# Kernel tuning notes

Measured on AMD Instinct MI355X. Metric: run time of the kernel, lower is better.

Reference implementation:

```python
import jax, jax.numpy as jnp
import numpy as np

LOSS_ALPHA = 0.7  # Config.loss_alpha


def setup_inputs() -> dict:
    key = jax.random.key(0)
    k1, k2, k3 = jax.random.split(key, 3)
    N, D, K = 1024, 256, 65536
    online_emb = jax.random.normal(k1, (N, D), dtype=jnp.float32)
    mom_emb = jax.random.normal(k2, (N, D), dtype=jnp.float32)
    queue = jax.random.normal(k3, (D, K), dtype=jnp.float32)
    temp = jnp.full((1,), 0.07, dtype=jnp.float32)
    return {"online_emb": online_emb, "mom_emb": mom_emb, "queue": queue, "temp": temp}


def _ce_label0(logits):
    # cross-entropy with target class 0 for every row, mean over batch
    return jnp.mean(jax.nn.logsumexp(logits, axis=1) - logits[:, 0])


def reference(online_emb, mom_emb, queue, temp):
    pos_sim = jnp.einsum('nd,nd->n', online_emb, mom_emb)          # [N]
    neg_sim = jnp.einsum('nd,dk->nk', online_emb, queue)           # [N, K]
    logits_raw = jnp.concatenate([pos_sim[:, None], neg_sim], axis=1)  # [N, K+1]
    t = temp[0]
    loss_online = _ce_label0(logits_raw / t)
    loss_momentum = _ce_label0(logits_raw / jax.lax.stop_gradient(t))
    return LOSS_ALPHA * loss_online + (1.0 - LOSS_ALPHA) * loss_momentum
```

## Files before the change

### kernel.cpp

```cpp
#include <hip/hip_runtime.h>
#include <hip/hip_bf16.h>


#define NROWS 1024
#define DDIM  256
#define KQ    65536
#define BN    128
#define NPART 512
#define LN2_F 0.69314718055994531f

typedef short  short8  __attribute__((ext_vector_type(8)));
typedef float  floatx4 __attribute__((ext_vector_type(4)));

__device__ __forceinline__ unsigned short f2bf(float f) {
    unsigned int u = __float_as_uint(f);
    u += 0x7FFFu + ((u >> 16) & 1u);
    return (unsigned short)(u >> 16);
}

#define DPPMOV(x, ctrl) \
    __uint_as_float(__builtin_amdgcn_mov_dpp(__float_as_uint(x), (ctrl), 0xF, 0xF, true))

__device__ __forceinline__ float dpp16_max(float x) {
    x = fmaxf(x, DPPMOV(x, 0xB1));
    x = fmaxf(x, DPPMOV(x, 0x4E));
    x = fmaxf(x, DPPMOV(x, 0x141));
    x = fmaxf(x, DPPMOV(x, 0x140));
    return x;
}
__device__ __forceinline__ float dpp16_sum(float x) {
    x += DPPMOV(x, 0xB1);
    x += DPPMOV(x, 0x4E);
    x += DPPMOV(x, 0x141);
    x += DPPMOV(x, 0x140);
    return x;
}

__global__ __launch_bounds__(256)
void conv_a(const float* __restrict__ A, const float* __restrict__ temp,
            unsigned short* __restrict__ Ab, float* __restrict__ out)
{
    if (blockIdx.x == 0 && threadIdx.x == 0) out[0] = 0.0f;
    const float s = 1.0f / (temp[0] * LN2_F);
    const int i = blockIdx.x * 256 + threadIdx.x;
    const floatx4 v = ((const floatx4*)A)[i];
    ushort4 w;
    w.x = f2bf(v.x * s); w.y = f2bf(v.y * s);
    w.z = f2bf(v.z * s); w.w = f2bf(v.w * s);
    ((ushort4*)Ab)[i] = w;
}

__global__ __launch_bounds__(256, 2)
void gemm_softmax(const unsigned short* __restrict__ Ab,
                  const float* __restrict__ Q,
                  float2* __restrict__ partials)
{
    __shared__ __align__(16) unsigned short Bl[BN * DDIM];

    const int tid  = threadIdx.x;
    const int lane = tid & 63;
    const int wave = tid >> 6;
    const int l15  = lane & 15;
    const int quad = lane >> 4;
    const int nb   = blockIdx.x;
    const int nbase = nb * BN;

    #pragma unroll
    for (int iter = 0; iter < 4; ++iter) {
        const int t2 = iter * 256 + tid;
        const int ny = t2 & 31;
        const int ko = t2 >> 5;
        floatx4 v[8];
        #pragma unroll
        for (int j = 0; j < 8; ++j)
            v[j] = __builtin_nontemporal_load(
                       (const floatx4*)(Q + (size_t)(ko * 8 + j) * KQ + nbase + ny * 4));
        #pragma unroll
        for (int i2 = 0; i2 < 4; ++i2) {
            const int n = ny * 4 + i2;
            const int phys = ko ^ (n & 15);
            short8 w;
            #pragma unroll
            for (int j = 0; j < 8; ++j)
                w[j] = (short)f2bf(v[j][i2]);
            *(short8*)&Bl[n * DDIM + phys * 8] = w;
        }
    }
    __syncthreads();

    #pragma unroll 1
    for (int g = 0; g < 4; ++g) {
        const int rowbase = g * 256 + wave * 64;
        const unsigned short* apb = Ab + (size_t)(rowbase + l15) * DDIM + quad * 8;

        floatx4 acc[4][8] = {};
        short8 afA[4], afB[4], bfA[8], bfB[8];

        #pragma unroll
        for (int i = 0; i < 4; ++i)
            afA[i] = *(const short8*)(apb + i * 16 * DDIM);
        {
            const int vb = l15 * 512 + ((quad ^ l15) * 16);
            #pragma unroll
            for (int j = 0; j < 8; ++j)
                bfA[j] = *(const short8*)((const char*)Bl + vb + j * 8192);
        }

        #pragma unroll 1
        for (int sp = 0; sp < 4; ++sp) {
            const int s1 = 2 * sp + 1;
            #pragma unroll
            for (int i = 0; i < 4; ++i)
                afB[i] = *(const short8*)(apb + i * 16 * DDIM + s1 * 32);
            {
                const int vb = l15 * 512 + (((4 * s1 + quad) ^ l15) * 16);
                #pragma unroll
                for (int j = 0; j < 8; ++j)
                    bfB[j] = *(const short8*)((const char*)Bl + vb + j * 8192);
            }
            #pragma unroll
            for (int i = 0; i < 4; ++i)
                #pragma unroll
                for (int j = 0; j < 8; ++j)
                    acc[i][j] = __builtin_amdgcn_mfma_f32_16x16x32_bf16(afA[i], bfA[j], acc[i][j], 0, 0, 0);

            const int s2 = (2 * sp + 2) & 7;
            #pragma unroll
            for (int i = 0; i < 4; ++i)
                afA[i] = *(const short8*)(apb + i * 16 * DDIM + s2 * 32);
            {
                const int vb = l15 * 512 + (((4 * s2 + quad) ^ l15) * 16);
                #pragma unroll
                for (int j = 0; j < 8; ++j)
                    bfA[j] = *(const short8*)((const char*)Bl + vb + j * 8192);
            }
            #pragma unroll
            for (int i = 0; i < 4; ++i)
                #pragma unroll
                for (int j = 0; j < 8; ++j)
                    acc[i][j] = __builtin_amdgcn_mfma_f32_16x16x32_bf16(afB[i], bfB[j], acc[i][j], 0, 0, 0);
        }

        #pragma unroll
        for (int i = 0; i < 4; ++i) {
            float2 tmp[4];
            #pragma unroll
            for (int r = 0; r < 4; ++r) {
                float mx = acc[i][0][r];
                #pragma unroll
                for (int j = 1; j < 8; ++j) mx = fmaxf(mx, acc[i][j][r]);
                mx = dpp16_max(mx);
                float s2 = 0.f;
                #pragma unroll
                for (int j = 0; j < 8; ++j)
                    s2 += __builtin_amdgcn_exp2f(acc[i][j][r] - mx);
                s2 = dpp16_sum(s2);
                tmp[r] = make_float2(mx, s2);
            }
            if (l15 == 0) {
                const int row = rowbase + i * 16 + quad * 4;
                floatx4* dst = (floatx4*)(partials + (size_t)nb * NROWS + row);
                floatx4 w0 = {tmp[0].x, tmp[0].y, tmp[1].x, tmp[1].y};
                floatx4 w1 = {tmp[2].x, tmp[2].y, tmp[3].x, tmp[3].y};
                __builtin_nontemporal_store(w0, dst);
                __builtin_nontemporal_store(w1, dst + 1);
            }
        }
    }
}

__global__ __launch_bounds__(256)
void finalize_rows(const float2* __restrict__ partials,
                   const float* __restrict__ online,
                   const float* __restrict__ mom,
                   const float* __restrict__ temp,
                   float* __restrict__ out)
{
    const int t = threadIdx.x;
    __shared__ float2 sm[16][17];
    __shared__ float sm_pos[16];

    {
        const float s = 1.0f / (temp[0] * LN2_F);
        const int r2 = t >> 4, c2 = t & 15;
        const float* po = online + (size_t)(blockIdx.x * 16 + r2) * DDIM + c2 * 16;
        const float* pm = mom    + (size_t)(blockIdx.x * 16 + r2) * DDIM + c2 * 16;
        float d = 0.f;
        #pragma unroll
        for (int w = 0; w < 4; ++w) {
            const floatx4 a = *(const floatx4*)(po + w * 4);
            const floatx4 b = *(const floatx4*)(pm + w * 4);
            d += a.x * b.x + a.y * b.y + a.z * b.z + a.w * b.w;
        }
        d = dpp16_sum(d);
        if (c2 == 0) sm_pos[r2] = d * s;
    }

    const int rl  = t & 15;
    const int grp = t >> 4;
    const int row = blockIdx.x * 16 + rl;

    float M = -3.0e38f, S = 0.f;
    #pragma unroll 1
    for (int pb = 0; pb < 32; pb += 8) {
        float2 v[8];
        #pragma unroll
        for (int j = 0; j < 8; ++j)
            v[j] = partials[(size_t)(grp * 32 + pb + j) * NROWS + row];
        #pragma unroll
        for (int j = 0; j < 8; ++j) {
            const float M2 = fmaxf(M, v[j].x);
            S = S * __builtin_amdgcn_exp2f(M - M2) + v[j].y * __builtin_amdgcn_exp2f(v[j].x - M2);
            M = M2;
        }
    }
    sm[grp][rl] = make_float2(M, S);
    __syncthreads();

    if (t < 64) {
        float val = 0.f;
        if (t < 16) {
            float Mm = -3.0e38f, Ss = 0.f;
            #pragma unroll
            for (int g2 = 0; g2 < 16; ++g2) {
                const float2 v = sm[g2][t];
                const float M2 = fmaxf(Mm, v.x);
                Ss = Ss * __builtin_amdgcn_exp2f(Mm - M2) + v.y * __builtin_amdgcn_exp2f(v.x - M2);
                Mm = M2;
            }
            const float p  = sm_pos[t];
            const float M2 = fmaxf(Mm, p);
            const float L  = Ss * __builtin_amdgcn_exp2f(Mm - M2) + __builtin_amdgcn_exp2f(p - M2);
            val = (M2 + __builtin_amdgcn_logf(L) - p) * LN2_F;
        }
        val += __shfl_xor(val, 1, 64);
        val += __shfl_xor(val, 2, 64);
        val += __shfl_xor(val, 4, 64);
        val += __shfl_xor(val, 8, 64);
        val += __shfl_xor(val, 16, 64);
        val += __shfl_xor(val, 32, 64);
        if (t == 0) atomicAdd(out, val * (1.0f / (float)NROWS));
    }
}

extern "C" void kernel_launch(void* const* d_in, const int* in_sizes, int n_in,
                              void* d_out, int out_size, void* d_ws, size_t ws_size,
                              hipStream_t stream)
{
    const float* online = (const float*)d_in[0];
    const float* mom    = (const float*)d_in[1];
    const float* queue  = (const float*)d_in[2];
    const float* temp   = (const float*)d_in[3];
    float* out = (float*)d_out;

    char* ws = (char*)d_ws;
    unsigned short* Ab = (unsigned short*)ws;
    float2* partials   = (float2*)(ws + 524288);

    conv_a<<<256, 256, 0, stream>>>(online, temp, Ab, out);
    gemm_softmax<<<KQ / BN, 256, 0, stream>>>(Ab, queue, partials);
    finalize_rows<<<64, 256, 0, stream>>>(partials, online, mom, temp, out);
}
```

Baseline: 150.9 us.

## Switch to 32x32x16 MFMA with 64-column queue tiles and more blocks

Halves the queue tile width to 64 columns, doubling the grid to 1024 blocks and the partials count, and replaces the 16x16x32 MFMA tiling with 32x32x16 MFMA on 2x2 accumulator tiles per wave. The occupancy target rises to 3 blocks per CU, helped by less shared memory per block. The intent is better CU load balance and a cheaper per-wave fragment footprint. The trade-offs are twice as many partials for the finalize kernel to merge, extra cross-half shuffles in the softmax epilogue, and less B-tile reuse per block.

```diff
diff --git a/kernel.cpp b/kernel.cpp
--- a/kernel.cpp
+++ b/kernel.cpp
@@ -5,12 +5,13 @@
 #define NROWS 1024
 #define DDIM  256
 #define KQ    65536
-#define BN    128
-#define NPART 512
+#define BN    64
+#define NPART 1024
 #define LN2_F 0.69314718055994531f
 
-typedef short  short8  __attribute__((ext_vector_type(8)));
-typedef float  floatx4 __attribute__((ext_vector_type(4)));
+typedef short  short8   __attribute__((ext_vector_type(8)));
+typedef float  floatx4  __attribute__((ext_vector_type(4)));
+typedef float  floatx16 __attribute__((ext_vector_type(16)));
 
 __device__ __forceinline__ unsigned short f2bf(float f) {
     unsigned int u = __float_as_uint(f);
@@ -50,7 +51,7 @@
     ((ushort4*)Ab)[i] = w;
 }
 
-__global__ __launch_bounds__(256, 2)
+__global__ __launch_bounds__(256, 3)
 void gemm_softmax(const unsigned short* __restrict__ Ab,
                   const float* __restrict__ Q,
                   float2* __restrict__ partials)
@@ -60,16 +61,17 @@
     const int tid  = threadIdx.x;
     const int lane = tid & 63;
     const int wave = tid >> 6;
+    const int l31  = lane & 31;
     const int l15  = lane & 15;
-    const int quad = lane >> 4;
+    const int half = lane >> 5;
     const int nb   = blockIdx.x;
     const int nbase = nb * BN;
 
     #pragma unroll
-    for (int iter = 0; iter < 4; ++iter) {
+    for (int iter = 0; iter < 2; ++iter) {
         const int t2 = iter * 256 + tid;
-        const int ny = t2 & 31;
-        const int ko = t2 >> 5;
+        const int ny = t2 & 15;
+        const int ko = t2 >> 4;
         floatx4 v[8];
         #pragma unroll
         for (int j = 0; j < 8; ++j)
@@ -88,82 +90,78 @@
     }
     __syncthreads();
 
+    const int nA = l31 * 512;
+    const int nB = (32 + l31) * 512;
+
     #pragma unroll 1
     for (int g = 0; g < 4; ++g) {
         const int rowbase = g * 256 + wave * 64;
-        const unsigned short* apb = Ab + (size_t)(rowbase + l15) * DDIM + quad * 8;
-
-        floatx4 acc[4][8] = {};
-        short8 afA[4], afB[4], bfA[8], bfB[8];
-
-        #pragma unroll
-        for (int i = 0; i < 4; ++i)
-            afA[i] = *(const short8*)(apb + i * 16 * DDIM);
+        const unsigned short* apb = Ab + (size_t)(rowbase + l31) * DDIM + half * 8;
+
+        floatx16 acc[2][2] = {};
+        short8 afA[2], afB[2], bfA[2], bfB[2];
+
+        afA[0] = *(const short8*)(apb);
+        afA[1] = *(const short8*)(apb + 32 * DDIM);
         {
-            const int vb = l15 * 512 + ((quad ^ l15) * 16);
+            const int off = ((half ^ l15) * 16);
+            bfA[0] = *(const short8*)((const char*)Bl + nA + off);
+            bfA[1] = *(const short8*)((const char*)Bl + nB + off);
+        }
+
+        #pragma unroll 1
+        for (int sp = 0; sp < 8; ++sp) {
+            const int s1 = 2 * sp + 1;
+            afB[0] = *(const short8*)(apb + s1 * 16);
+            afB[1] = *(const short8*)(apb + 32 * DDIM + s1 * 16);
+            {
+                const int off = (((2 * s1 + half) ^ l15) * 16);
+                bfB[0] = *(const short8*)((const char*)Bl + nA + off);
+                bfB[1] = *(const short8*)((const char*)Bl + nB + off);
+            }
+            acc[0][0] = __builtin_amdgcn_mfma_f32_32x32x16_bf16(afA[0], bfA[0], acc[0][0], 0, 0, 0);
+            acc[0][1] = __builtin_amdgcn_mfma_f32_32x32x16_bf16(afA[0], bfA[1], acc[0][1], 0, 0, 0);
+            acc[1][0] = __builtin_amdgcn_mfma_f32_32x32x16_bf16(afA[1], bfA[0], acc[1][0], 0, 0, 0);
+            acc[1][1] = __builtin_amdgcn_mfma_f32_32x32x16_bf16(afA[1], bfA[1], acc[1][1], 0, 0, 0);
+
+            const int s2 = (2 * sp + 2) & 15;
+            afA[0] = *(const short8*)(apb + s2 * 16);
+            afA[1] = *(const short8*)(apb + 32 * DDIM + s2 * 16);
+            {
+                const int off = (((2 * s2 + half) ^ l15) * 16);
+                bfA[0] = *(const short8*)((const char*)Bl + nA + off);
+                bfA[1] = *(const short8*)((const char*)Bl + nB + off);
+            }
+            acc[0][0] = __builtin_amdgcn_mfma_f32_32x32x16_bf16(afB[0], bfB[0], acc[0][0], 0, 0, 0);
+            acc[0][1] = __builtin_amdgcn_mfma_f32_32x32x16_bf16(afB[0], bfB[1], acc[0][1], 0, 0, 0);
+            acc[1][0] = __builtin_amdgcn_mfma_f32_32x32x16_bf16(afB[1], bfB[0], acc[1][0], 0, 0, 0);
+            acc[1][1] = __builtin_amdgcn_mfma_f32_32x32x16_bf16(afB[1], bfB[1], acc[1][1], 0, 0, 0);
+        }
+
+        #pragma unroll
+        for (int ti = 0; ti < 2; ++ti) {
+            float2 vals[16];
             #pragma unroll
-            for (int j = 0; j < 8; ++j)
-                bfA[j] = *(const short8*)((const char*)Bl + vb + j * 8192);
-        }
-
-        #pragma unroll 1
-        for (int sp = 0; sp < 4; ++sp) {
-            const int s1 = 2 * sp + 1;
-            #pragma unroll
-            for (int i = 0; i < 4; ++i)
-                afB[i] = *(const short8*)(apb + i * 16 * DDIM + s1 * 32);
-            {
-                const int vb = l15 * 512 + (((4 * s1 + quad) ^ l15) * 16);
+            for (int reg = 0; reg < 16; ++reg) {
+                float mx = fmaxf(acc[ti][0][reg], acc[ti][1][reg]);
+                mx = dpp16_max(mx);
+                mx = fmaxf(mx, __shfl_xor(mx, 16, 64));
+                float s2 = __builtin_amdgcn_exp2f(acc[ti][0][reg] - mx)
+                         + __builtin_amdgcn_exp2f(acc[ti][1][reg] - mx);
+                s2 = dpp16_sum(s2);
+                s2 += __shfl_xor(s2, 16, 64);
+                vals[reg] = make_float2(mx, s2);
+            }
+            if (l31 == 0) {
+                const int rb0 = rowbase + ti * 32 + 4 * half;
+                float2* dst = partials + (size_t)nb * NROWS + rb0;
                 #pragma unroll
-                for (int j = 0; j < 8; ++j)
-                    bfB[j] = *(const short8*)((const char*)Bl + vb + j * 8192);
-            }
-            #pragma unroll
-            for (int i = 0; i < 4; ++i)
-                #pragma unroll
-                for (int j = 0; j < 8; ++j)
-                    acc[i][j] = __builtin_amdgcn_mfma_f32_16x16x32_bf16(afA[i], bfA[j], acc[i][j], 0, 0, 0);
-
-            const int s2 = (2 * sp + 2) & 7;
-            #pragma unroll
-            for (int i = 0; i < 4; ++i)
-                afA[i] = *(const short8*)(apb + i * 16 * DDIM + s2 * 32);
-            {
-                const int vb = l15 * 512 + (((4 * s2 + quad) ^ l15) * 16);
-                #pragma unroll
-                for (int j = 0; j < 8; ++j)
-                    bfA[j] = *(const short8*)((const char*)Bl + vb + j * 8192);
-            }
-            #pragma unroll
-            for (int i = 0; i < 4; ++i)
-                #pragma unroll
-                for (int j = 0; j < 8; ++j)
-                    acc[i][j] = __builtin_amdgcn_mfma_f32_16x16x32_bf16(afB[i], bfB[j], acc[i][j], 0, 0, 0);
-        }
-
-        #pragma unroll
-        for (int i = 0; i < 4; ++i) {
-            float2 tmp[4];
-            #pragma unroll
-            for (int r = 0; r < 4; ++r) {
-                float mx = acc[i][0][r];
-                #pragma unroll
-                for (int j = 1; j < 8; ++j) mx = fmaxf(mx, acc[i][j][r]);
-                mx = dpp16_max(mx);
-                float s2 = 0.f;
-                #pragma unroll
-                for (int j = 0; j < 8; ++j)
-                    s2 += __builtin_amdgcn_exp2f(acc[i][j][r] - mx);
-                s2 = dpp16_sum(s2);
-                tmp[r] = make_float2(mx, s2);
-            }
-            if (l15 == 0) {
-                const int row = rowbase + i * 16 + quad * 4;
-                floatx4* dst = (floatx4*)(partials + (size_t)nb * NROWS + row);
-                floatx4 w0 = {tmp[0].x, tmp[0].y, tmp[1].x, tmp[1].y};
-                floatx4 w1 = {tmp[2].x, tmp[2].y, tmp[3].x, tmp[3].y};
-                __builtin_nontemporal_store(w0, dst);
-                __builtin_nontemporal_store(w1, dst + 1);
+                for (int q = 0; q < 4; ++q) {
+                    floatx4 w0 = {vals[q*4+0].x, vals[q*4+0].y, vals[q*4+1].x, vals[q*4+1].y};
+                    floatx4 w1 = {vals[q*4+2].x, vals[q*4+2].y, vals[q*4+3].x, vals[q*4+3].y};
+                    __builtin_nontemporal_store(w0, (floatx4*)(dst + q * 8));
+                    __builtin_nontemporal_store(w1, (floatx4*)(dst + q * 8 + 2));
+                }
             }
         }
     }
@@ -202,11 +200,11 @@
 
     float M = -3.0e38f, S = 0.f;
     #pragma unroll 1
-    for (int pb = 0; pb < 32; pb += 8) {
+    for (int pb = 0; pb < 64; pb += 8) {
         float2 v[8];
         #pragma unroll
         for (int j = 0; j < 8; ++j)
-            v[j] = partials[(size_t)(grp * 32 + pb + j) * NROWS + row];
+            v[j] = partials[(size_t)(grp * 64 + pb + j) * NROWS + row];
         #pragma unroll
         for (int j = 0; j < 8; ++j) {
             const float M2 = fmaxf(M, v[j].x);
```

After: 186.5 us. 23.6% more time.

## Switch GEMM operands from bf16 to fp8 e4m3 with smaller key tiles

Applied to the files above, without the earlier changes.

Converts the scaled online embeddings and the queue tile to FP8 E4M3 instead of BF16, and uses fp8 MFMA instructions for the similarity GEMM. It halves the key tile (BN 64), which halves shared-memory use and allows four blocks per CU. The shared-memory swizzle is adapted to 8-byte fp8 fragments. Partials per row double, so the finalize kernel reduces twice as many chunks. FP8 sharply reduces mantissa precision of the logits, which risks going beyond the accuracy tolerance of the loss.

```diff
diff --git a/kernel.cpp b/kernel.cpp
--- a/kernel.cpp
+++ b/kernel.cpp
@@ -1,21 +1,20 @@
 #include <hip/hip_runtime.h>
 #include <hip/hip_bf16.h>
+#include <hip/hip_fp8.h>
 
 
 #define NROWS 1024
 #define DDIM  256
 #define KQ    65536
-#define BN    128
-#define NPART 512
+#define BN    64
+#define NPART 1024
 #define LN2_F 0.69314718055994531f
 
-typedef short  short8  __attribute__((ext_vector_type(8)));
-typedef float  floatx4 __attribute__((ext_vector_type(4)));
-
-__device__ __forceinline__ unsigned short f2bf(float f) {
-    unsigned int u = __float_as_uint(f);
-    u += 0x7FFFu + ((u >> 16) & 1u);
-    return (unsigned short)(u >> 16);
+typedef float floatx4 __attribute__((ext_vector_type(4)));
+
+__device__ __forceinline__ unsigned char f2e4(float f) {
+    __hip_fp8_e4m3 t(f);
+    return (unsigned char)t.__x;
 }
 
 #define DPPMOV(x, ctrl) \
@@ -38,24 +37,25 @@
 
 __global__ __launch_bounds__(256)
 void conv_a(const float* __restrict__ A, const float* __restrict__ temp,
-            unsigned short* __restrict__ Ab, float* __restrict__ out)
+            unsigned char* __restrict__ Ab, float* __restrict__ out)
 {
     if (blockIdx.x == 0 && threadIdx.x == 0) out[0] = 0.0f;
     const float s = 1.0f / (temp[0] * LN2_F);
     const int i = blockIdx.x * 256 + threadIdx.x;
     const floatx4 v = ((const floatx4*)A)[i];
-    ushort4 w;
-    w.x = f2bf(v.x * s); w.y = f2bf(v.y * s);
-    w.z = f2bf(v.z * s); w.w = f2bf(v.w * s);
-    ((ushort4*)Ab)[i] = w;
-}
-
-__global__ __launch_bounds__(256, 2)
-void gemm_softmax(const unsigned short* __restrict__ Ab,
+    unsigned int w = (unsigned int)f2e4(v.x * s)
+                   | ((unsigned int)f2e4(v.y * s) << 8)
+                   | ((unsigned int)f2e4(v.z * s) << 16)
+                   | ((unsigned int)f2e4(v.w * s) << 24);
+    ((unsigned int*)Ab)[i] = w;
+}
+
+__global__ __launch_bounds__(256, 4)
+void gemm_softmax(const unsigned char* __restrict__ Ab,
                   const float* __restrict__ Q,
                   float2* __restrict__ partials)
 {
-    __shared__ __align__(16) unsigned short Bl[BN * DDIM];
+    __shared__ __align__(16) unsigned char Bl[BN * DDIM];
 
     const int tid  = threadIdx.x;
     const int lane = tid & 63;
@@ -66,10 +66,10 @@
     const int nbase = nb * BN;
 
     #pragma unroll
-    for (int iter = 0; iter < 4; ++iter) {
+    for (int iter = 0; iter < 2; ++iter) {
         const int t2 = iter * 256 + tid;
-        const int ny = t2 & 31;
-        const int ko = t2 >> 5;
+        const int ny = t2 & 15;
+        const int ko = t2 >> 4;
         floatx4 v[8];
         #pragma unroll
         for (int j = 0; j < 8; ++j)
@@ -78,12 +78,12 @@
         #pragma unroll
         for (int i2 = 0; i2 < 4; ++i2) {
             const int n = ny * 4 + i2;
-            const int phys = ko ^ (n & 15);
-            short8 w;
+            const int phys = (ko & 16) | ((ko ^ n) & 15);
+            unsigned long w = 0;
             #pragma unroll
             for (int j = 0; j < 8; ++j)
-                w[j] = (short)f2bf(v[j][i2]);
-            *(short8*)&Bl[n * DDIM + phys * 8] = w;
+                w |= (unsigned long)f2e4(v[j][i2]) << (8 * j);
+            *(unsigned long*)&Bl[n * DDIM + phys * 8] = w;
         }
     }
     __syncthreads();
@@ -91,19 +91,19 @@
     #pragma unroll 1
     for (int g = 0; g < 4; ++g) {
         const int rowbase = g * 256 + wave * 64;
-        const unsigned short* apb = Ab + (size_t)(rowbase + l15) * DDIM + quad * 8;
-
-        floatx4 acc[4][8] = {};
-        short8 afA[4], afB[4], bfA[8], bfB[8];
+        const unsigned char* apb = Ab + (size_t)(rowbase + l15) * DDIM + quad * 8;
+
+        floatx4 acc[4][4] = {};
+        long afA[4], afB[4], bfA[4], bfB[4];
 
         #pragma unroll
         for (int i = 0; i < 4; ++i)
-            afA[i] = *(const short8*)(apb + i * 16 * DDIM);
+            afA[i] = *(const long*)(apb + i * 16 * DDIM);
         {
-            const int vb = l15 * 512 + ((quad ^ l15) * 16);
-            #pragma unroll
-            for (int j = 0; j < 8; ++j)
-                bfA[j] = *(const short8*)((const char*)Bl + vb + j * 8192);
+            const int phys = (quad & 16) | ((quad ^ l15) & 15);
+            #pragma unroll
+            for (int j = 0; j < 4; ++j)
+                bfA[j] = *(const long*)&Bl[(j * 16 + l15) * DDIM + phys * 8];
         }
 
         #pragma unroll 1
@@ -111,34 +111,36 @@
             const int s1 = 2 * sp + 1;
             #pragma unroll
             for (int i = 0; i < 4; ++i)
-                afB[i] = *(const short8*)(apb + i * 16 * DDIM + s1 * 32);
+                afB[i] = *(const long*)(apb + i * 16 * DDIM + s1 * 32);
             {
-                const int vb = l15 * 512 + (((4 * s1 + quad) ^ l15) * 16);
-                #pragma unroll
-                for (int j = 0; j < 8; ++j)
-                    bfB[j] = *(const short8*)((const char*)Bl + vb + j * 8192);
-            }
-            #pragma unroll
-            for (int i = 0; i < 4; ++i)
-                #pragma unroll
-                for (int j = 0; j < 8; ++j)
-                    acc[i][j] = __builtin_amdgcn_mfma_f32_16x16x32_bf16(afA[i], bfA[j], acc[i][j], 0, 0, 0);
+                const int c = 4 * s1 + quad;
+                const int phys = (c & 16) | ((c ^ l15) & 15);
+                #pragma unroll
+                for (int j = 0; j < 4; ++j)
+                    bfB[j] = *(const long*)&Bl[(j * 16 + l15) * DDIM + phys * 8];
+            }
+            #pragma unroll
+            for (int i = 0; i < 4; ++i)
+                #pragma unroll
+                for (int j = 0; j < 4; ++j)
+                    acc[i][j] = __builtin_amdgcn_mfma_f32_16x16x32_fp8_fp8(afA[i], bfA[j], acc[i][j], 0, 0, 0);
 
             const int s2 = (2 * sp + 2) & 7;
             #pragma unroll
             for (int i = 0; i < 4; ++i)
-                afA[i] = *(const short8*)(apb + i * 16 * DDIM + s2 * 32);
+                afA[i] = *(const long*)(apb + i * 16 * DDIM + s2 * 32);
             {
-                const int vb = l15 * 512 + (((4 * s2 + quad) ^ l15) * 16);
-                #pragma unroll
-                for (int j = 0; j < 8; ++j)
-                    bfA[j] = *(const short8*)((const char*)Bl + vb + j * 8192);
-            }
-            #pragma unroll
-            for (int i = 0; i < 4; ++i)
-                #pragma unroll
-                for (int j = 0; j < 8; ++j)
-                    acc[i][j] = __builtin_amdgcn_mfma_f32_16x16x32_bf16(afB[i], bfB[j], acc[i][j], 0, 0, 0);
+                const int c = 4 * s2 + quad;
+                const int phys = (c & 16) | ((c ^ l15) & 15);
+                #pragma unroll
+                for (int j = 0; j < 4; ++j)
+                    bfA[j] = *(const long*)&Bl[(j * 16 + l15) * DDIM + phys * 8];
+            }
+            #pragma unroll
+            for (int i = 0; i < 4; ++i)
+                #pragma unroll
+                for (int j = 0; j < 4; ++j)
+                    acc[i][j] = __builtin_amdgcn_mfma_f32_16x16x32_fp8_fp8(afB[i], bfB[j], acc[i][j], 0, 0, 0);
         }
 
         #pragma unroll
@@ -146,13 +148,12 @@
             float2 tmp[4];
             #pragma unroll
             for (int r = 0; r < 4; ++r) {
-                float mx = acc[i][0][r];
-                #pragma unroll
-                for (int j = 1; j < 8; ++j) mx = fmaxf(mx, acc[i][j][r]);
+                float mx = fmaxf(fmaxf(acc[i][0][r], acc[i][1][r]),
+                                 fmaxf(acc[i][2][r], acc[i][3][r]));
                 mx = dpp16_max(mx);
                 float s2 = 0.f;
                 #pragma unroll
-                for (int j = 0; j < 8; ++j)
+                for (int j = 0; j < 4; ++j)
                     s2 += __builtin_amdgcn_exp2f(acc[i][j][r] - mx);
                 s2 = dpp16_sum(s2);
                 tmp[r] = make_float2(mx, s2);
@@ -202,11 +203,11 @@
 
     float M = -3.0e38f, S = 0.f;
     #pragma unroll 1
-    for (int pb = 0; pb < 32; pb += 8) {
+    for (int pb = 0; pb < 64; pb += 8) {
         float2 v[8];
         #pragma unroll
         for (int j = 0; j < 8; ++j)
-            v[j] = partials[(size_t)(grp * 32 + pb + j) * NROWS + row];
+            v[j] = partials[(size_t)(grp * 64 + pb + j) * NROWS + row];
         #pragma unroll
         for (int j = 0; j < 8; ++j) {
             const float M2 = fmaxf(M, v[j].x);
@@ -254,8 +255,8 @@
     float* out = (float*)d_out;
 
     char* ws = (char*)d_ws;
-    unsigned short* Ab = (unsigned short*)ws;
-    float2* partials   = (float2*)(ws + 524288);
+    unsigned char* Ab = (unsigned char*)ws;
+    float2* partials  = (float2*)(ws + 262144);
 
     conv_a<<<256, 256, 0, stream>>>(online, temp, Ab, out);
     gemm_softmax<<<KQ / BN, 256, 0, stream>>>(Ab, queue, partials);
```

Measured after the change: 176.8 us. +17.2%, slower.
